# Optimization experiments

Measured on AMD Instinct MI355X. Metric: run time of the kernel, lower is better.

## Reference

```python
import jax, jax.numpy as jnp
import numpy as np

N = 400000      # simplices (edges of the complexes)
E = 2400000     # nnz of each Laplacian
F_IN = 32
H = 64
KAPPA = 3
G = 512         # graphs in batch
N_OUT = 8
EPS = 1e-5


def spmm(edge_index, edge_values, x, n):
    # y[i] = sum_e val_e * x[j],  i = edge_index[0], j = edge_index[1]
    msg = edge_values[:, None] * x[edge_index[1]]
    return jax.ops.segment_sum(msg, edge_index[0], num_segments=n)


def sc_layer(x, li, lv, ui, uv, Wl, bl, Wu, bu, Wh, bh):
    # SCNN layer: z_low + z_up + z_har (aggr_x fused in)
    n = x.shape[0]
    z = x @ Wh + bh                       # harmonic / identity term
    xl = x
    for k in range(KAPPA):
        xl = spmm(li, lv, xl, n)          # L_low^{k+1} x
        z = z + xl @ Wl[k] + bl[k]
    xu = x
    for k in range(KAPPA):
        xu = spmm(ui, uv, xu, n)          # L_up^{k+1} x
        z = z + xu @ Wu[k] + bu[k]
    return z


def batch_norm(x, gamma, beta):
    mean = jnp.mean(x, axis=0)
    var = jnp.mean((x - mean) ** 2, axis=0)   # biased, as torch BN training
    return (x - mean) * jax.lax.rsqrt(var + EPS) * gamma + beta


def setup_inputs() -> dict:
    key = jax.random.key(0)
    ks = jax.random.split(key, 32)
    s_in = 1.0 / np.sqrt(F_IN)
    s_h = 1.0 / np.sqrt(H)
    inp = {
        "x": jax.random.normal(ks[0], (N, F_IN), jnp.float32),
        "lower_edge_index": jax.random.randint(ks[1], (2, E), 0, N),
        "lower_edge_values": jax.random.normal(ks[2], (E,), jnp.float32),
        "upper_edge_index": jax.random.randint(ks[3], (2, E), 0, N),
        "upper_edge_values": jax.random.normal(ks[4], (E,), jnp.float32),
        "batch_index": jnp.sort(jax.random.randint(ks[5], (N,), 0, G)),
        # layer 0 (F_IN -> H)
        "l0_Wl": jax.random.normal(ks[6], (KAPPA, F_IN, H), jnp.float32) * s_in,
        "l0_bl": jnp.zeros((KAPPA, H), jnp.float32),
        "l0_Wu": jax.random.normal(ks[7], (KAPPA, F_IN, H), jnp.float32) * s_in,
        "l0_bu": jnp.zeros((KAPPA, H), jnp.float32),
        "l0_Wh": jax.random.normal(ks[8], (F_IN, H), jnp.float32) * s_in,
        "l0_bh": jnp.zeros((H,), jnp.float32),
        # layer 1 (H -> H)
        "l1_Wl": jax.random.normal(ks[9], (KAPPA, H, H), jnp.float32) * s_h,
        "l1_bl": jnp.zeros((KAPPA, H), jnp.float32),
        "l1_Wu": jax.random.normal(ks[10], (KAPPA, H, H), jnp.float32) * s_h,
        "l1_bu": jnp.zeros((KAPPA, H), jnp.float32),
        "l1_Wh": jax.random.normal(ks[11], (H, H), jnp.float32) * s_h,
        "l1_bh": jnp.zeros((H,), jnp.float32),
        # batch norms
        "bn0_g": jnp.ones((H,), jnp.float32),
        "bn0_b": jnp.zeros((H,), jnp.float32),
        "bn1_g": jnp.ones((H,), jnp.float32),
        "bn1_b": jnp.zeros((H,), jnp.float32),
        # output MLP [2H, H, N_OUT]
        "mlp_W1": jax.random.normal(ks[12], (2 * H, H), jnp.float32) / np.sqrt(2 * H),
        "mlp_b1": jnp.zeros((H,), jnp.float32),
        "mlp_W2": jax.random.normal(ks[13], (H, N_OUT), jnp.float32) * s_h,
        "mlp_b2": jnp.zeros((N_OUT,), jnp.float32),
    }
    return inp


def reference(x, lower_edge_values, upper_edge_values,
              l0_Wl, l0_bl, l0_Wu, l0_bu, l0_Wh, l0_bh,
              l1_Wl, l1_bl, l1_Wu, l1_bu, l1_Wh, l1_bh,
              bn0_g, bn0_b, bn1_g, bn1_b,
              mlp_W1, mlp_b1, mlp_W2, mlp_b2,
              lower_edge_index, upper_edge_index, batch_index):
    li, ui, bi = lower_edge_index, upper_edge_index, batch_index
    lv, uv = lower_edge_values, upper_edge_values

    h = sc_layer(x, li, lv, ui, uv, l0_Wl, l0_bl, l0_Wu, l0_bu, l0_Wh, l0_bh)
    h = jax.nn.elu(batch_norm(h, bn0_g, bn0_b))
    h = sc_layer(h, li, lv, ui, uv, l1_Wl, l1_bl, l1_Wu, l1_bu, l1_Wh, l1_bh)
    h = jax.nn.elu(batch_norm(h, bn1_g, bn1_b))

    # global max pool + global mean pool per graph
    gmax = jax.ops.segment_max(h, bi, num_segments=G)
    gsum = jax.ops.segment_sum(h, bi, num_segments=G)
    cnt = jax.ops.segment_sum(jnp.ones((h.shape[0],), h.dtype), bi, num_segments=G)
    gmean = gsum / jnp.maximum(cnt, 1.0)[:, None]
    g = jax.nn.elu(jnp.concatenate([gmax, gmean], axis=1))  # [G, 2H]

    # MLP [2H -> H -> N_OUT]
    g = jax.nn.relu(g @ mlp_W1 + mlp_b1)
    return g @ mlp_W2 + mlp_b2
```

## Files before the change

### kernel.cpp

```cpp
#include <hip/hip_runtime.h>
#include <hip/hip_bf16.h>
#include <math.h>

#define N_SIMP 400000
#define E_NNZ  2400000
#define FIN    32
#define HDIM   64
#define KAPPA  3
#define G_NUM  512
#define NOUT   8
#define BN_EPS 1e-5

#define NDIG_HALF 391
#define NDIG      782
#define P1_EDGES  16384
#define P1_BLOCKS 293
#define P1_T      1024
#define P2_CAP    7168
#define P2_T      512
#define P2_ITERS  14

typedef __hip_bfloat16 bf16;
typedef _Float16 f16;
typedef short s8v __attribute__((ext_vector_type(8)));
typedef ushort u8v __attribute__((ext_vector_type(8)));
typedef _Float16 h8v __attribute__((ext_vector_type(8)));
typedef float f4v __attribute__((ext_vector_type(4)));

__device__ __forceinline__ float elu_f(float x) {
    return x > 0.f ? x : expm1f(x);
}
__device__ __forceinline__ float bf2f(ushort u) {
    return __uint_as_float(((unsigned int)u) << 16);
}
__device__ __forceinline__ ushort f2bf(float f) {
    bf16 h = (bf16)f;
    return *(ushort*)&h;
}


__global__ __launch_bounds__(P1_T) void p1_hist_kernel(const int* __restrict__ eiL,
                                                       const int* __restrict__ eiU,
                                                       int* __restrict__ cnt) {
    __shared__ int h[NDIG];
    int t = threadIdx.x;
    for (int j = t; j < NDIG; j += P1_T) h[j] = 0;
    __syncthreads();
    int base_i = blockIdx.x * P1_EDGES;
#pragma unroll 4
    for (int k = 0; k < P1_EDGES / P1_T; ++k) {
        int i = base_i + k * P1_T + t;
        if (i < 2 * E_NNZ) {
            int dd;
            if (i < E_NNZ) dd = eiL[i] >> 10;
            else           dd = NDIG_HALF + (eiU[i - E_NNZ] >> 10);
            atomicAdd(&h[dd], 1);
        }
    }
    __syncthreads();
    for (int j = t; j < NDIG; j += P1_T) cnt[blockIdx.x * NDIG + j] = h[j];
}

__global__ void bofs_kernel(const int* __restrict__ cnt, int* __restrict__ bofs) {
    __shared__ int sdata[256];
    int t = threadIdx.x;
    const int* src = cnt + blockIdx.x * NDIG;
    int* dst = bofs + blockIdx.x * NDIG;
    int base = t * 4;
    int v0 = (base + 0 < NDIG) ? src[base + 0] : 0;
    int v1 = (base + 1 < NDIG) ? src[base + 1] : 0;
    int v2 = (base + 2 < NDIG) ? src[base + 2] : 0;
    int v3 = (base + 3 < NDIG) ? src[base + 3] : 0;
    int tsum = v0 + v1 + v2 + v3;
    sdata[t] = tsum;
    __syncthreads();
    for (int off = 1; off < 256; off <<= 1) {
        int x = (t >= off) ? sdata[t - off] : 0;
        __syncthreads();
        sdata[t] += x;
        __syncthreads();
    }
    int run = sdata[t] - tsum;
    if (base + 0 < NDIG) { dst[base + 0] = run; } run += v0;
    if (base + 1 < NDIG) { dst[base + 1] = run; } run += v1;
    if (base + 2 < NDIG) { dst[base + 2] = run; } run += v2;
    if (base + 3 < NDIG) { dst[base + 3] = run; }
}

__global__ void digit_total_kernel(const int* __restrict__ cnt, int* __restrict__ tot) {
    int d = blockIdx.x * 256 + threadIdx.x;
    if (d >= NDIG) return;
    int run = 0;
    for (int b = 0; b < P1_BLOCKS; ++b) run += cnt[b * NDIG + d];
    tot[d] = run;
}

__global__ __launch_bounds__(1024) void scan_base_kernel(int* __restrict__ tot) {
    __shared__ int s[1024];
    int t = threadIdx.x;
    int v = (t < NDIG) ? tot[t] : 0;
    s[t] = v;
    __syncthreads();
    for (int off = 1; off < 1024; off <<= 1) {
        int x = (t >= off) ? s[t - off] : 0;
        __syncthreads();
        s[t] += x;
        __syncthreads();
    }
    if (t < NDIG) tot[t] = s[t] - v;
    if (t == 1023) tot[NDIG] = s[1023];
}

__global__ __launch_bounds__(P1_T) void p1_scatter_kernel(
        const int* __restrict__ eiL, const float* __restrict__ lv,
        const int* __restrict__ eiU, const float* __restrict__ uv,
        const int* __restrict__ bofsv, int2* __restrict__ coarse) {
    __shared__ int h[NDIG];
    int t = threadIdx.x;
    int bbase = blockIdx.x * NDIG;
    for (int j = t; j < NDIG; j += P1_T) h[j] = bofsv[bbase + j];
    __syncthreads();
    int base_i = blockIdx.x * P1_EDGES;
    int wbase = blockIdx.x * P1_EDGES;
#pragma unroll 4
    for (int k = 0; k < P1_EDGES / P1_T; ++k) {
        int i = base_i + k * P1_T + t;
        if (i < 2 * E_NNZ) {
            int row, col, dd;
            float val;
            if (i < E_NNZ) {
                row = eiL[i]; col = eiL[E_NNZ + i]; val = lv[i];
                dd = row >> 10;
            } else {
                int e = i - E_NNZ;
                row = eiU[e]; col = eiU[E_NNZ + e]; val = uv[e];
                dd = NDIG_HALF + (row >> 10);
            }
            int pos = wbase + atomicAdd(&h[dd], 1);
            coarse[pos] = make_int2(((row & 1023) << 22) | col, __float_as_int(val));
        }
    }
}


__global__ __launch_bounds__(P2_T) void p2_build_kernel(
        const int2* __restrict__ coarse, const int* __restrict__ ccnt,
        const int* __restrict__ bofsv, const int* __restrict__ basev,
        int* __restrict__ rpL, int* __restrict__ rpU,
        int2* __restrict__ edgeL, int2* __restrict__ edgeU) {
    __shared__ int pk[P2_CAP];
    __shared__ int vl[P2_CAP];
    __shared__ int hist[1024];
    __shared__ int sc[P2_T];
    __shared__ int fo[P1_BLOCKS];
    __shared__ int stot;
    int d = blockIdx.x;
    int t = threadIdx.x;
    int len = 0, ofs = 0;
    if (t < P1_BLOCKS) { len = ccnt[t * NDIG + d]; ofs = bofsv[t * NDIG + d]; }
    sc[t] = len;
    __syncthreads();
    for (int off = 1; off < P2_T; off <<= 1) {
        int x = (t >= off) ? sc[t - off] : 0;
        __syncthreads();
        sc[t] += x;
        __syncthreads();
    }
    if (t < P1_BLOCKS) { fo[t] = sc[t] - len; hist[t] = len; hist[512 + t] = ofs; }
    if (t == P1_BLOCKS - 1) stot = sc[t];
    __syncthreads();
    int sz = stot;
    if (sz > P2_CAP) sz = P2_CAP;
    int wv = t >> 6, lane = t & 63;
    for (int b = wv; b < P1_BLOCKS; b += P2_T / 64) {
        int L = hist[b], O = hist[512 + b], F = fo[b];
        const int2* sp = coarse + (size_t)b * P1_EDGES + O;
        for (int j = lane; j < L; j += 64) {
            int dst2 = F + j;
            if (dst2 < P2_CAP) {
                int2 r = sp[j];
                pk[dst2] = r.x;
                vl[dst2] = r.y;
            }
        }
    }
    __syncthreads();
    hist[t] = 0;
    hist[t + P2_T] = 0;
    __syncthreads();
    int myrank[P2_ITERS];
#pragma unroll
    for (int k = 0; k < P2_ITERS; ++k) {
        int j = k * P2_T + t;
        myrank[k] = (j < sz) ? atomicAdd(&hist[((unsigned)pk[j]) >> 22], 1) : 0;
    }
    __syncthreads();
    int h0 = hist[2 * t], h1 = hist[2 * t + 1];
    sc[t] = h0 + h1;
    __syncthreads();
    for (int off = 1; off < P2_T; off <<= 1) {
        int x = (t >= off) ? sc[t - off] : 0;
        __syncthreads();
        sc[t] += x;
        __syncthreads();
    }
    int pbase = sc[t] - (h0 + h1);
    __syncthreads();
    hist[2 * t] = pbase;
    hist[2 * t + 1] = pbase + h0;
    int which = (d >= NDIG_HALF);
    int lbase = basev[d] - (which ? E_NNZ : 0);
    int rowbase = (which ? d - NDIG_HALF : d) << 10;
    int* rp = which ? rpU : rpL;
    int r0 = rowbase + 2 * t, r1 = r0 + 1;
    if (r0 < N_SIMP) rp[r0] = lbase + pbase;
    if (r1 < N_SIMP) rp[r1] = lbase + pbase + h0;
    __syncthreads();
    int2* eout = which ? edgeU : edgeL;
#pragma unroll
    for (int k = 0; k < P2_ITERS; ++k) {
        int j = k * P2_T + t;
        if (j < sz) {
            unsigned p = (unsigned)pk[j];
            int pos = lbase + hist[p >> 22] + myrank[k];
            eout[pos] = make_int2((int)(p & 0x3FFFFF), vl[j]);
        }
    }
}


__global__ void combine_bias_kernel(const float* __restrict__ bh,
                                    const float* __restrict__ bl,
                                    const float* __restrict__ bu,
                                    float* __restrict__ out) {
    int h = threadIdx.x;
    float acc = bh[h];
    for (int k = 0; k < KAPPA; ++k) acc += bl[k * HDIM + h] + bu[k * HDIM + h];
    out[h] = acc;
}

__global__ void f32_to_bf16_kernel(const float* __restrict__ in, bf16* __restrict__ out) {
    int idx = blockIdx.x * 256 + threadIdx.x;
    float4 v = ((const float4*)in)[idx];
    ushort4 w;
    w.x = f2bf(v.x); w.y = f2bf(v.y); w.z = f2bf(v.z); w.w = f2bf(v.w);
    ((ushort4*)out)[idx] = w;
}

__global__ void wtrans_all_kernel(const float* __restrict__ s0, const float* __restrict__ s1,
                                  const float* __restrict__ s2, const float* __restrict__ s3,
                                  const float* __restrict__ s4, const float* __restrict__ s5,
                                  ushort* __restrict__ wt) {
    int idx = blockIdx.x * 256 + threadIdx.x;
    const float* src; int Ktot, off;
    if (idx < 2048)       { src = s0; Ktot = 32;  off = 0; }
    else if (idx < 6144)  { src = s1; Ktot = 64;  off = 2048; }
    else if (idx < 12288) { src = s2; Ktot = 96;  off = 6144; }
    else if (idx < 18432) { src = s3; Ktot = 96;  off = 12288; }
    else if (idx < 30720) { src = s4; Ktot = 192; off = 18432; }
    else                  { src = s5; Ktot = 192; off = 30720; }
    int rel = idx - off;
    int n = rel / Ktot, kk = rel - n * Ktot;
    wt[idx] = f2bf(src[kk * 64 + n]);
}


__global__ void spmm32_kernel(const int* __restrict__ rp, const int2* __restrict__ edge,
                              const bf16* __restrict__ srcb, int src_stride,
                              bf16* __restrict__ dstb) {
    const ushort* src = (const ushort*)srcb;
    ushort* dst = (ushort*)dstb;
    int tid = threadIdx.x;
    int lane = tid & 63;
    int wv = tid >> 6;
    int grp = lane >> 2;
    int li = lane & 3;
    int row = blockIdx.x * 64 + wv * 16 + grp;
    int s = rp[row];
    int e = (row == N_SIMP - 1) ? E_NNZ : rp[row + 1];
    int deg = e - s;
    float a[8] = {0.f, 0.f, 0.f, 0.f, 0.f, 0.f, 0.f, 0.f};
    if (deg > 0) {
        int2 ed[8];
#pragma unroll
        for (int t = 0; t < 8; ++t) {
            int j = s + t;
            ed[t] = edge[(j < e) ? j : (e - 1)];
        }
        u8v xs[8];
#pragma unroll
        for (int t = 0; t < 8; ++t)
            xs[t] = *(const u8v*)(src + (size_t)ed[t].x * src_stride + li * 8);
#pragma unroll
        for (int t = 0; t < 8; ++t) {
            float v = (t < deg) ? __int_as_float(ed[t].y) : 0.f;
#pragma unroll
            for (int c = 0; c < 8; ++c) a[c] += v * bf2f(xs[t][c]);
        }
        for (int j = s + 8; j < e; j += 4) {
            int2 e2[4];
#pragma unroll
            for (int t = 0; t < 4; ++t) {
                int jj = j + t;
                e2[t] = edge[(jj < e) ? jj : (e - 1)];
            }
            u8v x2[4];
#pragma unroll
            for (int t = 0; t < 4; ++t)
                x2[t] = *(const u8v*)(src + (size_t)e2[t].x * src_stride + li * 8);
#pragma unroll
            for (int t = 0; t < 4; ++t) {
                float v = (j + t < e) ? __int_as_float(e2[t].y) : 0.f;
#pragma unroll
                for (int c = 0; c < 8; ++c) a[c] += v * bf2f(x2[t][c]);
            }
        }
    }
    u8v w;
#pragma unroll
    for (int c = 0; c < 8; ++c) w[c] = f2bf(a[c]);
    *(u8v*)(dst + (size_t)row * 32 + li * 8) = w;
}

__global__ void spmm64_kernel(const int* __restrict__ rp, const int2* __restrict__ edge,
                              const bf16* __restrict__ srcb, bf16* __restrict__ dstb) {
    const ushort* src = (const ushort*)srcb;
    ushort* dst = (ushort*)dstb;
    int tid = threadIdx.x;
    int lane = tid & 63;
    int wv = tid >> 6;
    int grp = lane >> 3;
    int li = lane & 7;
    int row = blockIdx.x * 32 + wv * 8 + grp;
    int s = rp[row];
    int e = (row == N_SIMP - 1) ? E_NNZ : rp[row + 1];
    int deg = e - s;
    float a[8] = {0.f, 0.f, 0.f, 0.f, 0.f, 0.f, 0.f, 0.f};
    if (deg > 0) {
        int2 ed[8];
#pragma unroll
        for (int t = 0; t < 8; ++t) {
            int j = s + t;
            ed[t] = edge[(j < e) ? j : (e - 1)];
        }
        u8v xs[8];
#pragma unroll
        for (int t = 0; t < 8; ++t)
            xs[t] = *(const u8v*)(src + (size_t)ed[t].x * 64 + li * 8);
#pragma unroll
        for (int t = 0; t < 8; ++t) {
            float v = (t < deg) ? __int_as_float(ed[t].y) : 0.f;
#pragma unroll
            for (int c = 0; c < 8; ++c) a[c] += v * bf2f(xs[t][c]);
        }
        for (int j = s + 8; j < e; j += 4) {
            int2 e2[4];
#pragma unroll
            for (int t = 0; t < 4; ++t) {
                int jj = j + t;
                e2[t] = edge[(jj < e) ? jj : (e - 1)];
            }
            u8v x2[4];
#pragma unroll
            for (int t = 0; t < 4; ++t)
                x2[t] = *(const u8v*)(src + (size_t)e2[t].x * 64 + li * 8);
#pragma unroll
            for (int t = 0; t < 4; ++t) {
                float v = (j + t < e) ? __int_as_float(e2[t].y) : 0.f;
#pragma unroll
                for (int c = 0; c < 8; ++c) a[c] += v * bf2f(x2[t][c]);
            }
        }
    }
    u8v w;
#pragma unroll
    for (int c = 0; c < 8; ++c) w[c] = f2bf(a[c]);
    *(u8v*)(dst + (size_t)row * 64 + li * 8) = w;
}


template <int NCH, int NCH1, bool INIT>
__global__ __launch_bounds__(256) void mfma_gemm_kernel(
        const ushort* __restrict__ s0, int st0,
        const ushort* __restrict__ s1, int st1,
        const ushort* __restrict__ s2, int st2,
        const ushort* __restrict__ s3, int st3,
        const ushort* __restrict__ s4, int st4,
        const ushort* __restrict__ s5, int st5,
        const ushort* __restrict__ Wt1, int Kstride1,
        const ushort* __restrict__ Wt2, int Kstride2,
        const float* __restrict__ bias,
        f16* __restrict__ z) {
    int tid = threadIdx.x;
    int wv = tid >> 6, lane = tid & 63;
    int quad = lane >> 4, n = lane & 15;
    int rowbase = blockIdx.x * 64 + wv * 16;
    int arow = rowbase + n;

    f4v acc0 = {0.f, 0.f, 0.f, 0.f};
    f4v acc1 = {0.f, 0.f, 0.f, 0.f};
    f4v acc2 = {0.f, 0.f, 0.f, 0.f};
    f4v acc3 = {0.f, 0.f, 0.f, 0.f};

#pragma unroll
    for (int ch = 0; ch < NCH; ++ch) {
        const ushort* sp = (ch == 0) ? s0 : (ch == 1) ? s1 : (ch == 2) ? s2
                         : (ch == 3) ? s3 : (ch == 4) ? s4 : s5;
        int st = (ch == 0) ? st0 : (ch == 1) ? st1 : (ch == 2) ? st2
               : (ch == 3) ? st3 : (ch == 4) ? st4 : st5;
        const ushort* wb = (ch < NCH1) ? (Wt1 + ch * 32) : (Wt2 + (ch - NCH1) * 32);
        int Ks = (ch < NCH1) ? Kstride1 : Kstride2;
        s8v a = *(const s8v*)(sp + (size_t)arow * st + quad * 8);
        const ushort* wq = wb + quad * 8;
        s8v b0 = *(const s8v*)(wq + (size_t)(0 * 16 + n) * Ks);
        s8v b1 = *(const s8v*)(wq + (size_t)(1 * 16 + n) * Ks);
        s8v b2 = *(const s8v*)(wq + (size_t)(2 * 16 + n) * Ks);
        s8v b3 = *(const s8v*)(wq + (size_t)(3 * 16 + n) * Ks);
        acc0 = __builtin_amdgcn_mfma_f32_16x16x32_bf16(a, b0, acc0, 0, 0, 0);
        acc1 = __builtin_amdgcn_mfma_f32_16x16x32_bf16(a, b1, acc1, 0, 0, 0);
        acc2 = __builtin_amdgcn_mfma_f32_16x16x32_bf16(a, b2, acc2, 0, 0, 0);
        acc3 = __builtin_amdgcn_mfma_f32_16x16x32_bf16(a, b3, acc3, 0, 0, 0);
    }
#pragma unroll
    for (int r = 0; r < 4; ++r) {
        int orow = rowbase + quad * 4 + r;
        f16* zp = z + (size_t)orow * 64 + n;
        if (INIT) {
            zp[0]  = (f16)(bias[n]      + acc0[r]);
            zp[16] = (f16)(bias[16 + n] + acc1[r]);
            zp[32] = (f16)(bias[32 + n] + acc2[r]);
            zp[48] = (f16)(bias[48 + n] + acc3[r]);
        } else {
            zp[0]  = (f16)((float)zp[0]  + acc0[r]);
            zp[16] = (f16)((float)zp[16] + acc1[r]);
            zp[32] = (f16)((float)zp[32] + acc2[r]);
            zp[48] = (f16)((float)zp[48] + acc3[r]);
        }
    }
}


__global__ void bn_stats_kernel(const f16* __restrict__ z, double* __restrict__ stats) {
    __shared__ float ss[256 * 8], qq[256 * 8];
    int tid = threadIdx.x;
    const h8v* z8 = (const h8v*)z;
    const int total8 = N_SIMP * HDIM / 8;
    float fs[8] = {0, 0, 0, 0, 0, 0, 0, 0};
    float fq[8] = {0, 0, 0, 0, 0, 0, 0, 0};
    for (int i = blockIdx.x * 256 + tid; i < total8; i += (int)gridDim.x * 256) {
        h8v v = z8[i];
#pragma unroll
        for (int c = 0; c < 8; ++c) {
            float f = (float)v[c];
            fs[c] += f;
            fq[c] += f * f;
        }
    }
#pragma unroll
    for (int c = 0; c < 8; ++c) { ss[tid * 8 + c] = fs[c]; qq[tid * 8 + c] = fq[c]; }
    __syncthreads();
    if (tid < 64) {
        int sel = tid >> 3, slot = tid & 7;
        double a = 0.0, b = 0.0;
#pragma unroll 8
        for (int k = 0; k < 32; ++k) {
            int t = sel + (k << 3);
            a += (double)ss[t * 8 + slot];
            b += (double)qq[t * 8 + slot];
        }
        atomicAdd(&stats[tid], a);
        atomicAdd(&stats[64 + tid], b);
    }
}

__global__ void bn_elu_bf16_kernel(const f16* __restrict__ z, const double* __restrict__ stats,
                                   const float* __restrict__ gamma, const float* __restrict__ beta,
                                   bf16* __restrict__ out) {
    __shared__ float scale_s[64], shift_s[64];
    int tid = threadIdx.x;
    if (tid < 64) {
        double mean = stats[tid] / (double)N_SIMP;
        double var = stats[64 + tid] / (double)N_SIMP - mean * mean;
        double sc = (double)gamma[tid] / sqrt(var + BN_EPS);
        scale_s[tid] = (float)sc;
        shift_s[tid] = (float)((double)beta[tid] - mean * sc);
    }
    __syncthreads();
    const h8v* z8 = (const h8v*)z;
    u8v* o8 = (u8v*)out;
    const int total8 = N_SIMP * HDIM / 8;
    int hb = (tid & 7) * 8;
    for (int i = blockIdx.x * 256 + tid; i < total8; i += (int)gridDim.x * 256) {
        h8v v = z8[i];
        u8v w;
#pragma unroll
        for (int c = 0; c < 8; ++c)
            w[c] = f2bf(elu_f((float)v[c] * scale_s[hb + c] + shift_s[hb + c]));
        o8[i] = w;
    }
}

__global__ void bn_elu_f16_kernel(f16* __restrict__ z, const double* __restrict__ stats,
                                  const float* __restrict__ gamma, const float* __restrict__ beta) {
    __shared__ float scale_s[64], shift_s[64];
    int tid = threadIdx.x;
    if (tid < 64) {
        double mean = stats[tid] / (double)N_SIMP;
        double var = stats[64 + tid] / (double)N_SIMP - mean * mean;
        double sc = (double)gamma[tid] / sqrt(var + BN_EPS);
        scale_s[tid] = (float)sc;
        shift_s[tid] = (float)((double)beta[tid] - mean * sc);
    }
    __syncthreads();
    h8v* z8 = (h8v*)z;
    const int total8 = N_SIMP * HDIM / 8;
    int hb = (tid & 7) * 8;
    for (int i = blockIdx.x * 256 + tid; i < total8; i += (int)gridDim.x * 256) {
        h8v v = z8[i];
        h8v w;
#pragma unroll
        for (int c = 0; c < 8; ++c)
            w[c] = (f16)elu_f((float)v[c] * scale_s[hb + c] + shift_s[hb + c]);
        z8[i] = w;
    }
}

__global__ void pool_kernel(const f16* __restrict__ hbuf, const int* __restrict__ bidx,
                            float* __restrict__ gbuf) {
    __shared__ float smax[256], ssum[256];
    int g = blockIdx.x;
    int tid = threadIdx.x;
    int lo = 0, hi = N_SIMP;
    while (lo < hi) { int mid = (lo + hi) >> 1; if (bidx[mid] < g) lo = mid + 1; else hi = mid; }
    int start = lo;
    hi = N_SIMP;
    while (lo < hi) { int mid = (lo + hi) >> 1; if (bidx[mid] < g + 1) lo = mid + 1; else hi = mid; }
    int end = lo;
    int h = tid & 63, rep = tid >> 6;
    float mx = -INFINITY, sm = 0.f;
    for (int i = start + rep; i < end; i += 4) {
        float v = (float)hbuf[(size_t)i * HDIM + h];
        mx = fmaxf(mx, v);
        sm += v;
    }
    smax[tid] = mx; ssum[tid] = sm;
    __syncthreads();
    if (tid < 64) {
        float m = fmaxf(fmaxf(smax[tid], smax[tid + 64]), fmaxf(smax[tid + 128], smax[tid + 192]));
        float s = ssum[tid] + ssum[tid + 64] + ssum[tid + 128] + ssum[tid + 192];
        int cnt = end - start;
        float mean = s / fmaxf((float)cnt, 1.f);
        gbuf[g * 128 + tid] = elu_f(m);
        gbuf[g * 128 + 64 + tid] = elu_f(mean);
    }
}

__global__ void mlp_kernel(const float* __restrict__ gbuf, const float* __restrict__ W1,
                           const float* __restrict__ b1, const float* __restrict__ W2,
                           const float* __restrict__ b2, float* __restrict__ out) {
    __shared__ float gs[128];
    __shared__ float hs[64];
    int g = blockIdx.x, tid = threadIdx.x;
    gs[tid] = gbuf[g * 128 + tid];
    gs[64 + tid] = gbuf[g * 128 + 64 + tid];
    __syncthreads();
    float acc = b1[tid];
#pragma unroll
    for (int k = 0; k < 128; ++k) acc += gs[k] * W1[k * 64 + tid];
    hs[tid] = fmaxf(acc, 0.f);
    __syncthreads();
    if (tid < 8) {
        float o = b2[tid];
#pragma unroll
        for (int k = 0; k < 64; ++k) o += hs[k] * W2[k * 8 + tid];
        out[g * 8 + tid] = o;
    }
}


extern "C" void kernel_launch(void* const* d_in, const int* in_sizes, int n_in,
                              void* d_out, int out_size, void* d_ws, size_t ws_size,
                              hipStream_t stream) {
    const float* x     = (const float*)d_in[0];
    const int*   li    = (const int*)d_in[1];
    const float* lv    = (const float*)d_in[2];
    const int*   ui    = (const int*)d_in[3];
    const float* uv    = (const float*)d_in[4];
    const int*   bidx  = (const int*)d_in[5];
    const float* l0_Wl = (const float*)d_in[6];
    const float* l0_bl = (const float*)d_in[7];
    const float* l0_Wu = (const float*)d_in[8];
    const float* l0_bu = (const float*)d_in[9];
    const float* l0_Wh = (const float*)d_in[10];
    const float* l0_bh = (const float*)d_in[11];
    const float* l1_Wl = (const float*)d_in[12];
    const float* l1_bl = (const float*)d_in[13];
    const float* l1_Wu = (const float*)d_in[14];
    const float* l1_bu = (const float*)d_in[15];
    const float* l1_Wh = (const float*)d_in[16];
    const float* l1_bh = (const float*)d_in[17];
    const float* bn0_g = (const float*)d_in[18];
    const float* bn0_b = (const float*)d_in[19];
    const float* bn1_g = (const float*)d_in[20];
    const float* bn1_b = (const float*)d_in[21];
    const float* mW1   = (const float*)d_in[22];
    const float* mb1   = (const float*)d_in[23];
    const float* mW2   = (const float*)d_in[24];
    const float* mb2   = (const float*)d_in[25];
    float* out = (float*)d_out;

    char* base = (char*)d_ws;
    f16*   z     = (f16*)base;
    bf16*  h0bf  = (bf16*)(base + 51200000ull);
    bf16*  g1    = (bf16*)(base + 102400000ull);
    bf16*  g2    = (bf16*)(base + 153600000ull);
    int2*  edgeL = (int2*)(base + 204800000ull);
    int2*  edgeU = (int2*)(base + 224000000ull);
    int*   rpL   = (int*)(base + 243200000ull);
    int*   rpU   = (int*)(base + 244800032ull);
    double* stats = (double*)(base + 246404160ull);
    float* cbias  = (float*)(base + 246405184ull);
    float* gbuf   = (float*)(base + 246405440ull);
    ushort* wt    = (ushort*)(base + 246667584ull);

    int2* coarse = (int2*)base;
    int*  basev  = (int*)(base + 38500000ull);
    int*  ccnt   = (int*)(base + 51200000ull);
    int*  bofsv  = (int*)(base + 52200000ull);

    bf16* xbf  = g1;
    bf16* cAL  = g1 + (size_t)N_SIMP * 32;
    bf16* cBL  = g2;
    bf16* cCL  = g2 + (size_t)N_SIMP * 32;
    bf16* cAU  = h0bf;
    bf16* cBU  = h0bf + (size_t)N_SIMP * 32;
    bf16* cCU  = g1;

    ushort* wt_l0h = wt;
    ushort* wt_l1h = wt + 2048;
    ushort* wt_l0l = wt + 6144;
    ushort* wt_l0u = wt + 12288;
    ushort* wt_l1l = wt + 18432;
    ushort* wt_l1u = wt + 30720;

    const int SP32_BLOCKS = N_SIMP / 64;
    const int SP64_BLOCKS = N_SIMP / 32;
    const int MF_BLOCKS   = N_SIMP / 64;

    wtrans_all_kernel<<<168, 256, 0, stream>>>(l0_Wh, l1_Wh, l0_Wl, l0_Wu, l1_Wl, l1_Wu, wt);
    f32_to_bf16_kernel<<<N_SIMP * 32 / 4 / 256, 256, 0, stream>>>(x, xbf);

    p1_hist_kernel<<<P1_BLOCKS, P1_T, 0, stream>>>(li, ui, ccnt);
    bofs_kernel<<<P1_BLOCKS, 256, 0, stream>>>(ccnt, bofsv);
    digit_total_kernel<<<(NDIG + 255) / 256, 256, 0, stream>>>(ccnt, basev);
    scan_base_kernel<<<1, 1024, 0, stream>>>(basev);
    p1_scatter_kernel<<<P1_BLOCKS, P1_T, 0, stream>>>(li, lv, ui, uv, bofsv, coarse);
    p2_build_kernel<<<NDIG, P2_T, 0, stream>>>(coarse, ccnt, bofsv, basev,
                                               rpL, rpU, edgeL, edgeU);

    const ushort* xbfu = (const ushort*)xbf;
    const ushort* h0u  = (const ushort*)h0bf;
    const ushort* g1u  = (const ushort*)g1;
    const ushort* g2u  = (const ushort*)g2;

    combine_bias_kernel<<<1, 64, 0, stream>>>(l0_bh, l0_bl, l0_bu, cbias);
    mfma_gemm_kernel<1, 1, true><<<MF_BLOCKS, 256, 0, stream>>>(
        xbfu, 32, nullptr, 0, nullptr, 0, nullptr, 0, nullptr, 0, nullptr, 0,
        wt_l0h, 32, wt_l0h, 32, cbias, z);

    spmm32_kernel<<<SP32_BLOCKS, 256, 0, stream>>>(rpL, edgeL, xbf, 32, cAL);
    spmm32_kernel<<<SP32_BLOCKS, 256, 0, stream>>>(rpL, edgeL, cAL, 32, cBL);
    spmm32_kernel<<<SP32_BLOCKS, 256, 0, stream>>>(rpL, edgeL, cBL, 32, cCL);
    spmm32_kernel<<<SP32_BLOCKS, 256, 0, stream>>>(rpU, edgeU, xbf, 32, cAU);
    spmm32_kernel<<<SP32_BLOCKS, 256, 0, stream>>>(rpU, edgeU, cAU, 32, cBU);
    spmm32_kernel<<<SP32_BLOCKS, 256, 0, stream>>>(rpU, edgeU, cBU, 32, cCU);
    mfma_gemm_kernel<6, 3, false><<<MF_BLOCKS, 256, 0, stream>>>(
        (const ushort*)cAL, 32, (const ushort*)cBL, 32, (const ushort*)cCL, 32,
        (const ushort*)cAU, 32, (const ushort*)cBU, 32, (const ushort*)cCU, 32,
        wt_l0l, 96, wt_l0u, 96, nullptr, z);

    (void)hipMemsetAsync(stats, 0, 128 * sizeof(double), stream);
    bn_stats_kernel<<<1024, 256, 0, stream>>>(z, stats);
    bn_elu_bf16_kernel<<<1024, 256, 0, stream>>>(z, stats, bn0_g, bn0_b, h0bf);

    combine_bias_kernel<<<1, 64, 0, stream>>>(l1_bh, l1_bl, l1_bu, cbias);
    mfma_gemm_kernel<2, 2, true><<<MF_BLOCKS, 256, 0, stream>>>(
        h0u, 64, h0u + 32, 64, nullptr, 0, nullptr, 0, nullptr, 0, nullptr, 0,
        wt_l1h, 64, wt_l1h, 64, cbias, z);

    spmm64_kernel<<<SP64_BLOCKS, 256, 0, stream>>>(rpL, edgeL, h0bf, g1);
    spmm64_kernel<<<SP64_BLOCKS, 256, 0, stream>>>(rpL, edgeL, g1, g2);
    mfma_gemm_kernel<4, 4, false><<<MF_BLOCKS, 256, 0, stream>>>(
        g1u, 64, g1u + 32, 64, g2u, 64, g2u + 32, 64, nullptr, 0, nullptr, 0,
        wt_l1l, 192, wt_l1l, 192, nullptr, z);
    spmm64_kernel<<<SP64_BLOCKS, 256, 0, stream>>>(rpL, edgeL, g2, g1);
    spmm64_kernel<<<SP64_BLOCKS, 256, 0, stream>>>(rpU, edgeU, h0bf, g2);
    mfma_gemm_kernel<4, 2, false><<<MF_BLOCKS, 256, 0, stream>>>(
        g1u, 64, g1u + 32, 64, g2u, 64, g2u + 32, 64, nullptr, 0, nullptr, 0,
        wt_l1l + 128, 192, wt_l1u, 192, nullptr, z);
    spmm64_kernel<<<SP64_BLOCKS, 256, 0, stream>>>(rpU, edgeU, g2, g1);
    spmm64_kernel<<<SP64_BLOCKS, 256, 0, stream>>>(rpU, edgeU, g1, g2);
    mfma_gemm_kernel<4, 4, false><<<MF_BLOCKS, 256, 0, stream>>>(
        g1u, 64, g1u + 32, 64, g2u, 64, g2u + 32, 64, nullptr, 0, nullptr, 0,
        wt_l1u + 64, 192, wt_l1u + 64, 192, nullptr, z);

    (void)hipMemsetAsync(stats, 0, 128 * sizeof(double), stream);
    bn_stats_kernel<<<1024, 256, 0, stream>>>(z, stats);
    bn_elu_f16_kernel<<<1024, 256, 0, stream>>>(z, stats, bn1_g, bn1_b);

    pool_kernel<<<G_NUM, 256, 0, stream>>>(z, bidx, gbuf);
    mlp_kernel<<<G_NUM, 64, 0, stream>>>(gbuf, mW1, mb1, mW2, mb2, out);
}
```

Measured before the change: 1.438 ms.

## Fuse radix histogram, block scan and scatter into one local-sort kernel

Merges the per-block digit histogram, per-block offset scan and scatter passes into a single kernel. Each block keeps its 16K edge records in registers, scans its histogram locally, stages the sorted records in 128 KB of shared memory and writes them out contiguously. This drops two launches and a second read of the edge index and value arrays, and turns scattered global writes into coalesced ones. In exchange it uses a very large shared-memory footprint and heavy register use per block (one block per CU), which lowers occupancy.

Result: faster. 1.391 ms (-3.2%).

```diff
diff --git a/kernel.cpp b/kernel.cpp
--- a/kernel.cpp
+++ b/kernel.cpp
@@ -16,6 +16,7 @@
 #define P1_EDGES  16384
 #define P1_BLOCKS 293
 #define P1_T      1024
+#define P1_EPT    16
 #define P2_CAP    7168
 #define P2_T      512
 #define P2_ITERS  14
@@ -39,52 +40,69 @@
 }
 
 
-__global__ __launch_bounds__(P1_T) void p1_hist_kernel(const int* __restrict__ eiL,
-                                                       const int* __restrict__ eiU,
-                                                       int* __restrict__ cnt) {
+__global__ __launch_bounds__(P1_T, 1) void p1_sort_kernel(
+        const int* __restrict__ eiL, const float* __restrict__ lv,
+        const int* __restrict__ eiU, const float* __restrict__ uv,
+        int* __restrict__ ccnt, int* __restrict__ bofsv,
+        int2* __restrict__ coarse) {
+    __shared__ int2 rec[P1_EDGES];
     __shared__ int h[NDIG];
+    __shared__ int hscan[P1_T];
     int t = threadIdx.x;
     for (int j = t; j < NDIG; j += P1_T) h[j] = 0;
     __syncthreads();
     int base_i = blockIdx.x * P1_EDGES;
-#pragma unroll 4
-    for (int k = 0; k < P1_EDGES / P1_T; ++k) {
+    int key[P1_EPT], val[P1_EPT], dg[P1_EPT];
+#pragma unroll
+    for (int k = 0; k < P1_EPT; ++k) {
         int i = base_i + k * P1_T + t;
+        int dd = -1;
         if (i < 2 * E_NNZ) {
-            int dd;
-            if (i < E_NNZ) dd = eiL[i] >> 10;
-            else           dd = NDIG_HALF + (eiU[i - E_NNZ] >> 10);
+            int row, col;
+            float v;
+            if (i < E_NNZ) {
+                row = eiL[i]; col = eiL[E_NNZ + i]; v = lv[i];
+                dd = row >> 10;
+            } else {
+                int e = i - E_NNZ;
+                row = eiU[e]; col = eiU[E_NNZ + e]; v = uv[e];
+                dd = NDIG_HALF + (row >> 10);
+            }
+            key[k] = ((row & 1023) << 22) | col;
+            val[k] = __float_as_int(v);
             atomicAdd(&h[dd], 1);
         }
-    }
-    __syncthreads();
-    for (int j = t; j < NDIG; j += P1_T) cnt[blockIdx.x * NDIG + j] = h[j];
-}
-
-__global__ void bofs_kernel(const int* __restrict__ cnt, int* __restrict__ bofs) {
-    __shared__ int sdata[256];
-    int t = threadIdx.x;
-    const int* src = cnt + blockIdx.x * NDIG;
-    int* dst = bofs + blockIdx.x * NDIG;
-    int base = t * 4;
-    int v0 = (base + 0 < NDIG) ? src[base + 0] : 0;
-    int v1 = (base + 1 < NDIG) ? src[base + 1] : 0;
-    int v2 = (base + 2 < NDIG) ? src[base + 2] : 0;
-    int v3 = (base + 3 < NDIG) ? src[base + 3] : 0;
-    int tsum = v0 + v1 + v2 + v3;
-    sdata[t] = tsum;
-    __syncthreads();
-    for (int off = 1; off < 256; off <<= 1) {
-        int x = (t >= off) ? sdata[t - off] : 0;
-        __syncthreads();
-        sdata[t] += x;
-        __syncthreads();
-    }
-    int run = sdata[t] - tsum;
-    if (base + 0 < NDIG) { dst[base + 0] = run; } run += v0;
-    if (base + 1 < NDIG) { dst[base + 1] = run; } run += v1;
-    if (base + 2 < NDIG) { dst[base + 2] = run; } run += v2;
-    if (base + 3 < NDIG) { dst[base + 3] = run; }
+        dg[k] = dd;
+    }
+    __syncthreads();
+    int cv = (t < NDIG) ? h[t] : 0;
+    hscan[t] = cv;
+    __syncthreads();
+    for (int off = 1; off < P1_T; off <<= 1) {
+        int x = (t >= off) ? hscan[t - off] : 0;
+        __syncthreads();
+        hscan[t] += x;
+        __syncthreads();
+    }
+    if (t < NDIG) {
+        int ex = hscan[t] - cv;
+        ccnt[blockIdx.x * NDIG + t] = cv;
+        bofsv[blockIdx.x * NDIG + t] = ex;
+        h[t] = ex;
+    }
+    __syncthreads();
+#pragma unroll
+    for (int k = 0; k < P1_EPT; ++k) {
+        if (dg[k] >= 0) {
+            int pos = atomicAdd(&h[dg[k]], 1);
+            rec[pos] = make_int2(key[k], val[k]);
+        }
+    }
+    __syncthreads();
+    int2* dst = coarse + (size_t)blockIdx.x * P1_EDGES;
+    int nrec = 2 * E_NNZ - base_i;
+    if (nrec > P1_EDGES) nrec = P1_EDGES;
+    for (int j = t; j < nrec; j += P1_T) dst[j] = rec[j];
 }
 
 __global__ void digit_total_kernel(const int* __restrict__ cnt, int* __restrict__ tot) {
@@ -109,37 +127,6 @@
     }
     if (t < NDIG) tot[t] = s[t] - v;
     if (t == 1023) tot[NDIG] = s[1023];
-}
-
-__global__ __launch_bounds__(P1_T) void p1_scatter_kernel(
-        const int* __restrict__ eiL, const float* __restrict__ lv,
-        const int* __restrict__ eiU, const float* __restrict__ uv,
-        const int* __restrict__ bofsv, int2* __restrict__ coarse) {
-    __shared__ int h[NDIG];
-    int t = threadIdx.x;
-    int bbase = blockIdx.x * NDIG;
-    for (int j = t; j < NDIG; j += P1_T) h[j] = bofsv[bbase + j];
-    __syncthreads();
-    int base_i = blockIdx.x * P1_EDGES;
-    int wbase = blockIdx.x * P1_EDGES;
-#pragma unroll 4
-    for (int k = 0; k < P1_EDGES / P1_T; ++k) {
-        int i = base_i + k * P1_T + t;
-        if (i < 2 * E_NNZ) {
-            int row, col, dd;
-            float val;
-            if (i < E_NNZ) {
-                row = eiL[i]; col = eiL[E_NNZ + i]; val = lv[i];
-                dd = row >> 10;
-            } else {
-                int e = i - E_NNZ;
-                row = eiU[e]; col = eiU[E_NNZ + e]; val = uv[e];
-                dd = NDIG_HALF + (row >> 10);
-            }
-            int pos = wbase + atomicAdd(&h[dd], 1);
-            coarse[pos] = make_int2(((row & 1023) << 22) | col, __float_as_int(val));
-        }
-    }
 }
 
 
@@ -650,11 +637,9 @@
     wtrans_all_kernel<<<168, 256, 0, stream>>>(l0_Wh, l1_Wh, l0_Wl, l0_Wu, l1_Wl, l1_Wu, wt);
     f32_to_bf16_kernel<<<N_SIMP * 32 / 4 / 256, 256, 0, stream>>>(x, xbf);
 
-    p1_hist_kernel<<<P1_BLOCKS, P1_T, 0, stream>>>(li, ui, ccnt);
-    bofs_kernel<<<P1_BLOCKS, 256, 0, stream>>>(ccnt, bofsv);
+    p1_sort_kernel<<<P1_BLOCKS, P1_T, 0, stream>>>(li, lv, ui, uv, ccnt, bofsv, coarse);
     digit_total_kernel<<<(NDIG + 255) / 256, 256, 0, stream>>>(ccnt, basev);
     scan_base_kernel<<<1, 1024, 0, stream>>>(basev);
-    p1_scatter_kernel<<<P1_BLOCKS, P1_T, 0, stream>>>(li, lv, ui, uv, bofsv, coarse);
     p2_build_kernel<<<NDIG, P2_T, 0, stream>>>(coarse, ccnt, bofsv, basev,
                                                rpL, rpU, edgeL, edgeU);
 
```
